# Kernel optimization log

Hardware: AMD Instinct MI355X
Metric: run time of the kernel (lower is better)

The kernel has to match this reference:

```python
import jax, jax.numpy as jnp
import numpy as np

N_NODES = 100000
D_FEAT = 256
INPUT_ATT = 256


def setup_inputs() -> dict:
    key = jax.random.key(0)
    k1, k2, k3, kw, kh = jax.random.split(key, 5)
    x1 = jax.random.normal(k1, (N_NODES, D_FEAT), dtype=jnp.float32)
    x2 = jax.random.normal(k2, (N_NODES, D_FEAT), dtype=jnp.float32)
    x3 = jax.random.normal(k3, (N_NODES, D_FEAT), dtype=jnp.float32)
    # xavier-normal-like init for parameters
    W = jax.random.normal(kw, (INPUT_ATT, N_NODES), dtype=jnp.float32) * float(np.sqrt(2.0 / (INPUT_ATT + N_NODES)))
    h_n = jax.random.normal(kh, (1, INPUT_ATT), dtype=jnp.float32) * float(np.sqrt(2.0 / (1 + INPUT_ATT)))
    return {"x1": x1, "x2": x2, "x3": x3, "W": W, "h_n": h_n}


def reference(x1, x2, x3, W, h_n):
    # temp_k = tanh(W @ x_k): (input_att, D) for each of the 3 views
    t1 = jnp.tanh(W @ x1)
    t2 = jnp.tanh(W @ x2)
    t3 = jnp.tanh(W @ x3)
    # per-view, per-feature score: (1, D) each -> stacked (3, D)
    scores = jnp.concatenate([h_n @ t1, h_n @ t2, h_n @ t3], axis=0)  # (3, D)
    beta = jax.nn.softmax(scores, axis=0)  # softmax over the 3 views, per feature column
    # fused broadcast weighted sum (replaces the per-row Python loop)
    out = beta[0] * x1 + beta[1] * x2 + beta[2] * x3  # (N, D)
    return out
```

## Files before the change

kernel.cpp:

```cpp
#include <hip/hip_runtime.h>
#include <hip/hip_bf16.h>

#define N_NODES 100000
#define D_FEAT  256
#define N_ATT   256

typedef __bf16 bf16x8 __attribute__((ext_vector_type(8)));
typedef float  f32x16 __attribute__((ext_vector_type(16)));

__device__ __forceinline__ unsigned short bf16_rne(float f) {
    unsigned u = __float_as_uint(f);
    return (unsigned short)((u + 0x7fffu + ((u >> 16) & 1u)) >> 16);
}

__device__ __forceinline__ void split1(float f, unsigned short& h, unsigned short& l) {
    h = bf16_rne(f);
    float fh = __uint_as_float((unsigned)h << 16);
    l = (unsigned short)(__float_as_uint(f - fh) >> 16);
}

#define LDK 40

__global__ __launch_bounds__(512, 4) void gemm_split(
    const float* __restrict__ x1, const float* __restrict__ x2,
    const float* __restrict__ x3, const float* __restrict__ W,
    float* __restrict__ C, int chunk)
{
    extern __shared__ unsigned short lds[];
    unsigned short* Ah = lds;
    unsigned short* Al = Ah + 128 * LDK;
    unsigned short* Bh = Al + 128 * LDK;
    unsigned short* Bl = Bh + 256 * LDK;

    const int bid = blockIdx.x;
    const int s   = bid / 6;
    const int pos = bid % 6;
    const int v   = pos >> 1;
    const int m0  = (pos & 1) * 128;
    const float* __restrict__ X = (v == 0) ? x1 : (v == 1) ? x2 : x3;

    const int ks = s * chunk;
    const int ke = min(ks + chunk, N_NODES);

    const int tid  = threadIdx.x;
    const int lane = tid & 63;
    const int wave = tid >> 6;
    const int mstrip = (wave & 3) * 32;
    const int nhalf  = (wave >> 2) * 128;

    const int a_m  = tid >> 3;
    const int a_kk = (tid & 7) * 4;
    const int b_n64 = tid & 63;
    const int b_nb  = (tid >> 8) * 64;
    const int b_kq  = ((tid >> 6) & 3) ^ ((tid >> 3) & 3);

    f32x16 acc[4] = {};

    const int l31 = lane & 31;
    const int khalf = (lane >> 5) * 8;

    for (int k0 = ks; k0 < ke; k0 += 32) {
        __syncthreads();

        #pragma unroll
        for (int p = 0; p < 2; ++p) {
            int m  = p * 64 + a_m;
            int kg = k0 + a_kk;
            float4 w4 = make_float4(0.f, 0.f, 0.f, 0.f);
            if (kg < ke)
                w4 = *(const float4*)(W + (size_t)(m0 + m) * N_NODES + kg);
            ushort4 h4, l4;
            split1(w4.x, h4.x, l4.x); split1(w4.y, h4.y, l4.y);
            split1(w4.z, h4.z, l4.z); split1(w4.w, h4.w, l4.w);
            *(ushort4*)(Ah + m * LDK + a_kk) = h4;
            *(ushort4*)(Al + m * LDK + a_kk) = l4;
        }
        #pragma unroll
        for (int p = 0; p < 4; ++p) {
            int n  = (p >> 1) * 128 + b_nb + b_n64;
            int kb = (p & 1) * 16 + b_kq * 4;
            int kg = k0 + kb;
            float e0 = 0.f, e1 = 0.f, e2 = 0.f, e3 = 0.f;
            if (kg < ke) {
                const float* xp = X + (size_t)kg * D_FEAT + n;
                e0 = xp[0]; e1 = xp[D_FEAT]; e2 = xp[2 * D_FEAT]; e3 = xp[3 * D_FEAT];
            }
            ushort4 h4, l4;
            split1(e0, h4.x, l4.x); split1(e1, h4.y, l4.y);
            split1(e2, h4.z, l4.z); split1(e3, h4.w, l4.w);
            *(ushort4*)(Bh + n * LDK + kb) = h4;
            *(ushort4*)(Bl + n * LDK + kb) = l4;
        }
        __syncthreads();

        #pragma unroll
        for (int kk = 0; kk < 2; ++kk) {
            int kf = kk * 16 + khalf;
            int arow = mstrip + l31;
            bf16x8 ah = *(bf16x8*)(Ah + arow * LDK + kf);
            bf16x8 al = *(bf16x8*)(Al + arow * LDK + kf);
            #pragma unroll
            for (int nb = 0; nb < 4; ++nb) {
                int brow = nhalf + nb * 32 + l31;
                bf16x8 bh = *(bf16x8*)(Bh + brow * LDK + kf);
                bf16x8 bl = *(bf16x8*)(Bl + brow * LDK + kf);
                acc[nb] = __builtin_amdgcn_mfma_f32_32x32x16_bf16(ah, bh, acc[nb], 0, 0, 0);
                acc[nb] = __builtin_amdgcn_mfma_f32_32x32x16_bf16(ah, bl, acc[nb], 0, 0, 0);
                acc[nb] = __builtin_amdgcn_mfma_f32_32x32x16_bf16(al, bh, acc[nb], 0, 0, 0);
            }
        }
    }

    float* Cv = C + v * (N_ATT * D_FEAT);
    const int col = l31;
    const int rbase = 4 * (lane >> 5);
    #pragma unroll
    for (int nb = 0; nb < 4; ++nb) {
        int gj = nhalf + nb * 32 + col;
        #pragma unroll
        for (int r = 0; r < 16; ++r) {
            int row = (r & 3) + 8 * (r >> 2) + rbase;
            int gi = m0 + mstrip + row;
            unsafeAtomicAdd(Cv + gi * D_FEAT + gj, acc[nb][r]);
        }
    }
}

__global__ __launch_bounds__(256) void score_kernel(
    const float* __restrict__ C, const float* __restrict__ h,
    float* __restrict__ scores)
{
    const int v  = blockIdx.x >> 3;
    const int ig = blockIdx.x & 7;
    const int j  = threadIdx.x;
    const float* Cv = C + v * (N_ATT * D_FEAT);
    float s = 0.f;
    #pragma unroll 4
    for (int i = ig * 32; i < ig * 32 + 32; ++i)
        s += h[i] * tanhf(Cv[i * D_FEAT + j]);
    unsafeAtomicAdd(scores + v * D_FEAT + j, s);
}

__device__ __forceinline__ float blend(float xa, float xb, float xc,
                                       float t0, float t1, float t2) {
    float m = fmaxf(t0, fmaxf(t1, t2));
    float e0 = __expf(t0 - m), e1 = __expf(t1 - m), e2 = __expf(t2 - m);
    float inv = 1.0f / (e0 + e1 + e2);
    return (e0 * xa + e1 * xb + e2 * xc) * inv;
}

__global__ __launch_bounds__(256) void out_kernel(
    const float* __restrict__ x1, const float* __restrict__ x2,
    const float* __restrict__ x3, const float* __restrict__ scores,
    float* __restrict__ out)
{
    size_t idx  = (size_t)blockIdx.x * 256 + threadIdx.x;
    size_t base = idx * 4;
    int j = (int)(base & (D_FEAT - 1));
    float4 a = *(const float4*)(x1 + base);
    float4 b = *(const float4*)(x2 + base);
    float4 c = *(const float4*)(x3 + base);
    float4 s0 = *(const float4*)(scores + j);
    float4 s1 = *(const float4*)(scores + D_FEAT + j);
    float4 s2 = *(const float4*)(scores + 2 * D_FEAT + j);
    float4 o;
    o.x = blend(a.x, b.x, c.x, s0.x, s1.x, s2.x);
    o.y = blend(a.y, b.y, c.y, s0.y, s1.y, s2.y);
    o.z = blend(a.z, b.z, c.z, s0.z, s1.z, s2.z);
    o.w = blend(a.w, b.w, c.w, s0.w, s1.w, s2.w);
    *(float4*)(out + base) = o;
}

extern "C" void kernel_launch(void* const* d_in, const int* in_sizes, int n_in,
                              void* d_out, int out_size, void* d_ws, size_t ws_size,
                              hipStream_t stream) {
    const float* x1 = (const float*)d_in[0];
    const float* x2 = (const float*)d_in[1];
    const float* x3 = (const float*)d_in[2];
    const float* W  = (const float*)d_in[3];
    const float* h  = (const float*)d_in[4];
    float* out = (float*)d_out;

    float* C      = (float*)d_ws;
    float* scores = C + 3 * N_ATT * D_FEAT;

    hipMemsetAsync(d_ws, 0, (3 * N_ATT * D_FEAT + 3 * D_FEAT) * sizeof(float), stream);

    const int chunk = 1180;
    gemm_split<<<dim3(510), dim3(512), 60 * 1024, stream>>>(x1, x2, x3, W, C, chunk);

    score_kernel<<<dim3(24), dim3(256), 0, stream>>>(C, h, scores);

    out_kernel<<<dim3((N_NODES * D_FEAT) / (4 * 256)), dim3(256), 0, stream>>>(
        x1, x2, x3, scores, out);
}
```

Before: 569.7 us.

## Prefetch next K-tile into registers and drop low-order split of X operand

```diff
diff --git a/kernel.cpp b/kernel.cpp
--- a/kernel.cpp
+++ b/kernel.cpp
@@ -5,6 +5,7 @@
 #define D_FEAT  256
 #define N_ATT   256
 
+typedef __bf16 bf16x4 __attribute__((ext_vector_type(4)));
 typedef __bf16 bf16x8 __attribute__((ext_vector_type(8)));
 typedef float  f32x16 __attribute__((ext_vector_type(16)));
 
@@ -19,7 +20,13 @@
     l = (unsigned short)(__float_as_uint(f - fh) >> 16);
 }
 
-#define LDK 40
+__device__ __forceinline__ bf16x8 ld8(const unsigned short* p) {
+    bf16x4 lo = *(const bf16x4*)p;
+    bf16x4 hi = *(const bf16x4*)(p + 4);
+    return __builtin_shufflevector(lo, hi, 0, 1, 2, 3, 4, 5, 6, 7);
+}
+
+#define LDK 36
 
 __global__ __launch_bounds__(512, 4) void gemm_split(
     const float* __restrict__ x1, const float* __restrict__ x2,
@@ -30,7 +37,6 @@
     unsigned short* Ah = lds;
     unsigned short* Al = Ah + 128 * LDK;
     unsigned short* Bh = Al + 128 * LDK;
-    unsigned short* Bl = Bh + 256 * LDK;
 
     const int bid = blockIdx.x;
     const int s   = bid / 6;
@@ -54,24 +60,48 @@
     const int b_nb  = (tid >> 8) * 64;
     const int b_kq  = ((tid >> 6) & 3) ^ ((tid >> 3) & 3);
 
-    f32x16 acc[4] = {};
-
     const int l31 = lane & 31;
     const int khalf = (lane >> 5) * 8;
 
+    f32x16 acc[4] = {};
+
+    float4 pa[2];
+    float  pb[4][4];
+
+    auto issue = [&](int kg0) {
+        #pragma unroll
+        for (int p = 0; p < 2; ++p) {
+            int kg = kg0 + a_kk;
+            pa[p] = make_float4(0.f, 0.f, 0.f, 0.f);
+            if (kg < ke)
+                pa[p] = *(const float4*)(W + (size_t)(m0 + p * 64 + a_m) * N_NODES + kg);
+        }
+        #pragma unroll
+        for (int p = 0; p < 4; ++p) {
+            int n  = (p >> 1) * 128 + b_nb + b_n64;
+            int kg = kg0 + (p & 1) * 16 + b_kq * 4;
+            pb[p][0] = pb[p][1] = pb[p][2] = pb[p][3] = 0.f;
+            if (kg < ke) {
+                const float* xp = X + (size_t)kg * D_FEAT + n;
+                pb[p][0] = xp[0];
+                pb[p][1] = xp[D_FEAT];
+                pb[p][2] = xp[2 * D_FEAT];
+                pb[p][3] = xp[3 * D_FEAT];
+            }
+        }
+    };
+
+    issue(ks);
+
     for (int k0 = ks; k0 < ke; k0 += 32) {
         __syncthreads();
 
         #pragma unroll
         for (int p = 0; p < 2; ++p) {
-            int m  = p * 64 + a_m;
-            int kg = k0 + a_kk;
-            float4 w4 = make_float4(0.f, 0.f, 0.f, 0.f);
-            if (kg < ke)
-                w4 = *(const float4*)(W + (size_t)(m0 + m) * N_NODES + kg);
             ushort4 h4, l4;
-            split1(w4.x, h4.x, l4.x); split1(w4.y, h4.y, l4.y);
-            split1(w4.z, h4.z, l4.z); split1(w4.w, h4.w, l4.w);
+            split1(pa[p].x, h4.x, l4.x); split1(pa[p].y, h4.y, l4.y);
+            split1(pa[p].z, h4.z, l4.z); split1(pa[p].w, h4.w, l4.w);
+            int m = p * 64 + a_m;
             *(ushort4*)(Ah + m * LDK + a_kk) = h4;
             *(ushort4*)(Al + m * LDK + a_kk) = l4;
         }
@@ -79,33 +109,27 @@
         for (int p = 0; p < 4; ++p) {
             int n  = (p >> 1) * 128 + b_nb + b_n64;
             int kb = (p & 1) * 16 + b_kq * 4;
-            int kg = k0 + kb;
-            float e0 = 0.f, e1 = 0.f, e2 = 0.f, e3 = 0.f;
-            if (kg < ke) {
-                const float* xp = X + (size_t)kg * D_FEAT + n;
-                e0 = xp[0]; e1 = xp[D_FEAT]; e2 = xp[2 * D_FEAT]; e3 = xp[3 * D_FEAT];
-            }
-            ushort4 h4, l4;
-            split1(e0, h4.x, l4.x); split1(e1, h4.y, l4.y);
-            split1(e2, h4.z, l4.z); split1(e3, h4.w, l4.w);
+            ushort4 h4;
+            h4.x = bf16_rne(pb[p][0]); h4.y = bf16_rne(pb[p][1]);
+            h4.z = bf16_rne(pb[p][2]); h4.w = bf16_rne(pb[p][3]);
             *(ushort4*)(Bh + n * LDK + kb) = h4;
-            *(ushort4*)(Bl + n * LDK + kb) = l4;
-        }
+        }
+
+        if (k0 + 32 < ke) issue(k0 + 32);
+
         __syncthreads();
 
         #pragma unroll
         for (int kk = 0; kk < 2; ++kk) {
             int kf = kk * 16 + khalf;
             int arow = mstrip + l31;
-            bf16x8 ah = *(bf16x8*)(Ah + arow * LDK + kf);
-            bf16x8 al = *(bf16x8*)(Al + arow * LDK + kf);
+            bf16x8 ah = ld8(Ah + arow * LDK + kf);
+            bf16x8 al = ld8(Al + arow * LDK + kf);
             #pragma unroll
             for (int nb = 0; nb < 4; ++nb) {
                 int brow = nhalf + nb * 32 + l31;
-                bf16x8 bh = *(bf16x8*)(Bh + brow * LDK + kf);
-                bf16x8 bl = *(bf16x8*)(Bl + brow * LDK + kf);
+                bf16x8 bh = ld8(Bh + brow * LDK + kf);
                 acc[nb] = __builtin_amdgcn_mfma_f32_32x32x16_bf16(ah, bh, acc[nb], 0, 0, 0);
-                acc[nb] = __builtin_amdgcn_mfma_f32_32x32x16_bf16(ah, bl, acc[nb], 0, 0, 0);
                 acc[nb] = __builtin_amdgcn_mfma_f32_32x32x16_bf16(al, bh, acc[nb], 0, 0, 0);
             }
         }
@@ -187,7 +211,7 @@
     hipMemsetAsync(d_ws, 0, (3 * N_ATT * D_FEAT + 3 * D_FEAT) * sizeof(float), stream);
 
     const int chunk = 1180;
-    gemm_split<<<dim3(510), dim3(512), 60 * 1024, stream>>>(x1, x2, x3, W, C, chunk);
+    gemm_split<<<dim3(510), dim3(512), 512 * LDK * 2, stream>>>(x1, x2, x3, W, C, chunk);
 
     score_kernel<<<dim3(24), dim3(256), 0, stream>>>(C, h, scores);
 
```

Result: faster. 505.5 us (-11.3%).
